# Kernel tuning notes

Hardware: AMD Instinct MI355X
Metric: run time of the kernel (lower is better)

Reference implementation:

```python
import jax, jax.numpy as jnp
import numpy as np

# ROIAlign config (torchvision semantics, aligned=False)
SPATIAL_SCALE = 0.25
POOLED = 7
SAMPLING_RATIO = 2
MODE = "max"  # from __init__ mode='max'


def setup_inputs() -> dict:
    key = jax.random.key(0)
    kf, kcx, kcy, kw, kh, kb = jax.random.split(key, 6)
    B, C, H, W = 2, 256, 200, 304
    N = 512
    IMG_H, IMG_W = H / SPATIAL_SCALE, W / SPATIAL_SCALE
    feature = jax.random.normal(kf, (B, C, H, W), dtype=jnp.float32)
    cx = jax.random.uniform(kcx, (N,)) * IMG_W
    cy = jax.random.uniform(kcy, (N,)) * IMG_H
    bw = jax.random.uniform(kw, (N,)) * 192.0 + 16.0
    bh = jax.random.uniform(kh, (N,)) * 192.0 + 16.0
    x1 = jnp.clip(cx - bw * 0.5, 0.0, IMG_W - 2.0)
    y1 = jnp.clip(cy - bh * 0.5, 0.0, IMG_H - 2.0)
    x2 = jnp.clip(cx + bw * 0.5, x1 + 1.0, IMG_W - 1.0)
    y2 = jnp.clip(cy + bh * 0.5, y1 + 1.0, IMG_H - 1.0)
    boxes = jnp.stack([x1, y1, x2, y2], axis=1).astype(jnp.float32)
    batch_idx = jax.random.randint(kb, (N,), 0, B, dtype=jnp.int32)
    return {"feature": feature, "boxes": boxes, "batch_idx": batch_idx}


def _sample_coords(start, size):
    # start,size: [N]; returns [N, POOLED*SAMPLING_RATIO] sample coordinates
    bin_sz = size / POOLED                         # [N]
    p = jnp.arange(POOLED, dtype=jnp.float32)      # bin index
    s = (jnp.arange(SAMPLING_RATIO, dtype=jnp.float32) + 0.5) / SAMPLING_RATIO
    # coord = start + (p + s) * bin_sz  -> [N, POOLED, RATIO]
    c = start[:, None, None] + (p[None, :, None] + s[None, None, :]) * bin_sz[:, None, None]
    return c.reshape(c.shape[0], POOLED * SAMPLING_RATIO)


def roi_align(feature, boxes, batch_idx):
    B, C, H, W = feature.shape
    roi = boxes * SPATIAL_SCALE                    # [N,4] in feature coords
    rs_x, rs_y, re_x, re_y = roi[:, 0], roi[:, 1], roi[:, 2], roi[:, 3]
    roi_w = jnp.maximum(re_x - rs_x, 1.0)
    roi_h = jnp.maximum(re_y - rs_y, 1.0)
    ys = _sample_coords(rs_y, roi_h)               # [N, Sy]
    xs = _sample_coords(rs_x, roi_w)               # [N, Sx]
    y = jnp.broadcast_to(ys[:, :, None], (ys.shape[0], ys.shape[1], xs.shape[1]))
    x = jnp.broadcast_to(xs[:, None, :], y.shape)  # [N, Sy, Sx]

    valid = (y > -1.0) & (y < H) & (x > -1.0) & (x < W)
    y = jnp.clip(y, 0.0, H - 1)
    x = jnp.clip(x, 0.0, W - 1)
    y0 = jnp.floor(y).astype(jnp.int32)
    x0 = jnp.floor(x).astype(jnp.int32)
    y1 = jnp.minimum(y0 + 1, H - 1)
    x1 = jnp.minimum(x0 + 1, W - 1)
    ly = y - y0.astype(y.dtype)
    lx = x - x0.astype(x.dtype)
    hy, hx = 1.0 - ly, 1.0 - lx
    b = batch_idx[:, None, None]
    # advanced indexing -> [N, Sy, Sx, C]
    val = (hy * hx)[..., None] * feature[b, :, y0, x0] \
        + (hy * lx)[..., None] * feature[b, :, y0, x1] \
        + (ly * hx)[..., None] * feature[b, :, y1, x0] \
        + (ly * lx)[..., None] * feature[b, :, y1, x1]
    val = jnp.where(valid[..., None], val, 0.0)
    N = boxes.shape[0]
    val = val.reshape(N, POOLED, SAMPLING_RATIO, POOLED, SAMPLING_RATIO, C)
    if MODE == "max":
        out = val.max(axis=(2, 4))                 # [N, PH, PW, C]
    else:
        out = val.mean(axis=(2, 4))
    return jnp.transpose(out, (0, 3, 1, 2))        # [N, C, PH, PW]


def reference(feature, boxes, batch_idx):
    return roi_align(feature, boxes, batch_idx)
```

## Files before the change

### kernel.cpp

```cpp
#include <hip/hip_runtime.h>


#define SPATIAL_SCALE 0.25f
#define POOLED 7
#define SR 2

constexpr int Bc = 2;
constexpr int Cc = 256;
constexpr int Hc = 200;
constexpr int Wc = 304;
constexpr int Nc = 512;

constexpr int CG      = 4;
constexpr int NSAMP   = POOLED * SR;
constexpr int NROW    = NSAMP * 2;
constexpr int XPAD    = 68;
constexpr int CH_STR  = NROW * XPAD;
constexpr int CELLS   = POOLED * POOLED;
constexpr int OUTS    = CG * CELLS;
constexpr int PER_BOX = Cc * CELLS;
constexpr int PLANE   = Hc * Wc;

constexpr int TB_F  = 1216;
constexpr int A_OFF = 784;
constexpr int R_OFF = 1176;
constexpr int X_OFF = 1204;
constexpr size_t TABLE_BYTES = (size_t)Nc * TB_F * sizeof(float);

__global__ __launch_bounds__(64) void roi_precompute_kernel(
    const float* __restrict__ boxes,
    float*       __restrict__ table)
{
    const int n   = blockIdx.x;
    const int tid = threadIdx.x;

    const float rsx = boxes[n * 4 + 0] * SPATIAL_SCALE;
    const float rsy = boxes[n * 4 + 1] * SPATIAL_SCALE;
    const float rex = boxes[n * 4 + 2] * SPATIAL_SCALE;
    const float rey = boxes[n * 4 + 3] * SPATIAL_SCALE;
    const float roi_w = fmaxf(rex - rsx, 1.0f);
    const float roi_h = fmaxf(rey - rsy, 1.0f);
    const float bin_w = roi_w / (float)POOLED;
    const float bin_h = roi_h / (float)POOLED;
    const float x_first = __fadd_rn(rsx, __fmul_rn(0.25f, bin_w));
    const float xc0     = fminf(fmaxf(x_first, 0.0f), (float)(Wc - 1));
    const int   xbase   = ((int)floorf(xc0)) & ~3;

    float* tb = table + (size_t)n * TB_F;
    int*   ti = (int*)tb;

    if (tid < CELLS) {
        const int ph = tid / POOLED;
        const int pw = tid - ph * POOLED;
        #pragma unroll
        for (int sy = 0; sy < SR; ++sy) {
            const int   sY  = ph * SR + sy;
            const float py  = (float)ph + ((float)sy + 0.5f) * 0.5f;
            const float fy  = __fadd_rn(rsy, __fmul_rn(py, bin_h));
            const bool  vy  = (fy > -1.0f) && (fy < (float)Hc);
            const float fyc = fminf(fmaxf(fy, 0.0f), (float)(Hc - 1));
            const int   y0i = (int)floorf(fyc);
            const float ly  = fyc - (float)y0i;
            const float hy  = 1.0f - ly;
            #pragma unroll
            for (int sx = 0; sx < SR; ++sx) {
                const float px  = (float)pw + ((float)sx + 0.5f) * 0.5f;
                const float fx  = __fadd_rn(rsx, __fmul_rn(px, bin_w));
                const bool  vx  = (fx > -1.0f) && (fx < (float)Wc);
                const float fxc = fminf(fmaxf(fx, 0.0f), (float)(Wc - 1));
                const int   x0i = (int)floorf(fxc);
                const float lx  = fxc - (float)x0i;
                const float hx  = 1.0f - lx;
                const int   c0  = x0i - xbase;
                const bool  v   = vy && vx;
                float4 w;
                w.x = v ? hy * hx : 0.0f;
                w.y = v ? hy * lx : 0.0f;
                w.z = v ? ly * hx : 0.0f;
                w.w = v ? ly * lx : 0.0f;
                const int tap = sy * SR + sx;
                ((float4*)tb)[tid * 4 + tap] = w;
                ti[A_OFF + tid * 8 + tap * 2 + 0] = sY * XPAD + c0;
                ti[A_OFF + tid * 8 + tap * 2 + 1] = (NSAMP + sY) * XPAD + c0;
            }
        }
    }
    if (tid < NROW) {
        const int which = tid / NSAMP;
        const int s     = tid - which * NSAMP;
        const int p     = s >> 1;
        const int sub   = s & 1;
        const float py  = (float)p + ((float)sub + 0.5f) * 0.5f;
        const float fy  = __fadd_rn(rsy, __fmul_rn(py, bin_h));
        const float fyc = fminf(fmaxf(fy, 0.0f), (float)(Hc - 1));
        const int   y0  = (int)floorf(fyc);
        const int   row = which ? min(y0 + 1, Hc - 1) : y0;
        ti[R_OFF + tid] = row * Wc;
    }
    if (tid == 0) ti[X_OFF] = xbase;
}

__global__ __launch_bounds__(256) void roi_align_main_kernel(
    const float* __restrict__ feature,
    const int*   __restrict__ batch_idx,
    const float* __restrict__ table,
    float*       __restrict__ out)
{
    __shared__ float lds[CG * CH_STR];

    const int bid = blockIdx.x;
    const int cg  = bid / Nc;
    const int n   = bid - cg * Nc;
    const int tid = threadIdx.x;

    const float* tb = table + (size_t)n * TB_F;
    const int*   ti = (const int*)tb;

    const int b     = batch_idx[n];
    const int xbase = ti[X_OFF];

    const int c_st   = tid >> 6;
    const int lane16 = tid & 15;
    const int rquad  = (tid >> 4) & 3;
    const int col    = min(xbase + lane16 * 4, Wc - 4);

    int roff[7];
    #pragma unroll
    for (int it = 0; it < 7; ++it)
        roff[it] = ti[R_OFF + it * 4 + rquad];

    const int cellc = min(tid, OUTS - 1);
    const int c_cl  = cellc / CELLS;
    const int cell  = cellc - c_cl * CELLS;
    const float4* wp = (const float4*)tb + (size_t)cell * 4;
    const float4 wv0 = wp[0], wv1 = wp[1], wv2 = wp[2], wv3 = wp[3];
    const int4* ap = (const int4*)(ti + A_OFF) + (size_t)cell * 2;
    const int4 av0 = ap[0], av1 = ap[1];

    const float* __restrict__ gbase =
        feature + ((size_t)b * Cc + (size_t)cg * CG + c_st) * (size_t)PLANE;
    float4 st[7];
    #pragma unroll
    for (int it = 0; it < 7; ++it)
        st[it] = *(const float4*)(gbase + roff[it] + col);

    const int lw = c_st * CH_STR + rquad * XPAD + lane16 * 4;
    #pragma unroll
    for (int it = 0; it < 7; ++it)
        *(float4*)&lds[lw + it * (4 * XPAD)] = st[it];

    __syncthreads();

    if (tid < OUTS) {
        const int lbase = c_cl * CH_STR;
        float m = -INFINITY;
        {   const int a0 = av0.x + lbase, a1 = av0.y + lbase;
            const float bil = wv0.x * lds[a0] + wv0.y * lds[a0 + 1]
                            + wv0.z * lds[a1] + wv0.w * lds[a1 + 1];
            m = fmaxf(m, bil); }
        {   const int a0 = av0.z + lbase, a1 = av0.w + lbase;
            const float bil = wv1.x * lds[a0] + wv1.y * lds[a0 + 1]
                            + wv1.z * lds[a1] + wv1.w * lds[a1 + 1];
            m = fmaxf(m, bil); }
        {   const int a0 = av1.x + lbase, a1 = av1.y + lbase;
            const float bil = wv2.x * lds[a0] + wv2.y * lds[a0 + 1]
                            + wv2.z * lds[a1] + wv2.w * lds[a1 + 1];
            m = fmaxf(m, bil); }
        {   const int a0 = av1.z + lbase, a1 = av1.w + lbase;
            const float bil = wv3.x * lds[a0] + wv3.y * lds[a0 + 1]
                            + wv3.z * lds[a1] + wv3.w * lds[a1 + 1];
            m = fmaxf(m, bil); }
        out[(size_t)n * PER_BOX + cg * OUTS + tid] = m;
    }
}

__global__ __launch_bounds__(256) void roi_align_max_fallback(
    const float* __restrict__ feature,
    const float* __restrict__ boxes,
    const int*   __restrict__ batch_idx,
    float*       __restrict__ out)
{
    __shared__ float lds[CG * CH_STR];

    int bid = blockIdx.x;
    int cg  = bid / Nc;
    int n   = bid - cg * Nc;
    int tid = threadIdx.x;

    float rsx = boxes[n * 4 + 0] * SPATIAL_SCALE;
    float rsy = boxes[n * 4 + 1] * SPATIAL_SCALE;
    float rex = boxes[n * 4 + 2] * SPATIAL_SCALE;
    float rey = boxes[n * 4 + 3] * SPATIAL_SCALE;
    float roi_w = fmaxf(rex - rsx, 1.0f);
    float roi_h = fmaxf(rey - rsy, 1.0f);
    float bin_w = roi_w / (float)POOLED;
    float bin_h = roi_h / (float)POOLED;
    int b = batch_idx[n];

    float x_first = __fadd_rn(rsx, __fmul_rn(0.25f, bin_w));
    float xc0 = fminf(fmaxf(x_first, 0.0f), (float)(Wc - 1));
    int xbase = ((int)floorf(xc0)) & ~3;

    const float* __restrict__ gbase =
        feature + ((size_t)b * Cc + (size_t)cg * CG) * (size_t)PLANE;

    int lane16 = tid & 15;
    int rbase  = tid >> 4;
    #pragma unroll
    for (int it = 0; it < 7; ++it) {
        int r       = it * 16 + rbase;
        int c_local = r / NROW;
        int slot    = r - c_local * NROW;
        int s       = slot % NSAMP;
        int which   = slot / NSAMP;
        int p       = s >> 1;
        int sub     = s & 1;
        float py = (float)p + ((float)sub + 0.5f) * 0.5f;
        float fy = __fadd_rn(rsy, __fmul_rn(py, bin_h));
        float fyc = fminf(fmaxf(fy, 0.0f), (float)(Hc - 1));
        int y0 = (int)floorf(fyc);
        int row = which ? min(y0 + 1, Hc - 1) : y0;
        int colf = min(xbase + lane16 * 4, Wc - 4);
        const float4 v = *(const float4*)(gbase + (size_t)c_local * PLANE
                                          + row * Wc + colf);
        *(float4*)&lds[c_local * CH_STR + slot * XPAD + lane16 * 4] = v;
    }
    __syncthreads();

    if (tid < OUTS) {
        int c_local = tid / CELLS;
        int cell    = tid - c_local * CELLS;
        int ph      = cell / POOLED;
        int pw      = cell - ph * POOLED;
        const float* __restrict__ L = &lds[c_local * CH_STR];

        float m = -INFINITY;
        #pragma unroll
        for (int sy = 0; sy < SR; ++sy) {
            int sY = ph * SR + sy;
            float py = (float)ph + ((float)sy + 0.5f) * 0.5f;
            float fy = __fadd_rn(rsy, __fmul_rn(py, bin_h));
            bool vy = (fy > -1.0f) && (fy < (float)Hc);
            float fyc = fminf(fmaxf(fy, 0.0f), (float)(Hc - 1));
            int y0 = (int)floorf(fyc);
            float ly = fyc - (float)y0;
            float hy = 1.0f - ly;
            const float* __restrict__ r0 = L + sY * XPAD;
            const float* __restrict__ r1 = L + (NSAMP + sY) * XPAD;

            #pragma unroll
            for (int sx = 0; sx < SR; ++sx) {
                float px = (float)pw + ((float)sx + 0.5f) * 0.5f;
                float fx = __fadd_rn(rsx, __fmul_rn(px, bin_w));
                bool vx = (fx > -1.0f) && (fx < (float)Wc);
                float fxc = fminf(fmaxf(fx, 0.0f), (float)(Wc - 1));
                int x0 = (int)floorf(fxc);
                float lx = fxc - (float)x0;
                float hx = 1.0f - lx;
                int c0 = x0 - xbase;

                float v00 = r0[c0], v01 = r0[c0 + 1];
                float v10 = r1[c0], v11 = r1[c0 + 1];
                float bil = hy * hx * v00 + hy * lx * v01 +
                            ly * hx * v10 + ly * lx * v11;
                float v = (vy && vx) ? bil : 0.0f;
                m = fmaxf(m, v);
            }
        }
        out[(size_t)n * PER_BOX + cg * OUTS + tid] = m;
    }
}

extern "C" void kernel_launch(void* const* d_in, const int* in_sizes, int n_in,
                              void* d_out, int out_size, void* d_ws, size_t ws_size,
                              hipStream_t stream) {
    const float* feature   = (const float*)d_in[0];
    const float* boxes     = (const float*)d_in[1];
    const int*   batch_idx = (const int*)d_in[2];
    float*       out       = (float*)d_out;

    const int grid = (Cc / CG) * Nc;
    if (d_ws != nullptr && ws_size >= TABLE_BYTES) {
        float* table = (float*)d_ws;
        roi_precompute_kernel<<<Nc, 64, 0, stream>>>(boxes, table);
        roi_align_main_kernel<<<grid, 256, 0, stream>>>(feature, batch_idx,
                                                        table, out);
    } else {
        roi_align_max_fallback<<<grid, 256, 0, stream>>>(feature, boxes,
                                                         batch_idx, out);
    }
}
```

Measured before the change: 255.4 us.

## Load only needed feature columns per ROI and recompute row offsets in-block

The main kernel now computes the x-span each ROI actually touches and skips the global float4 loads for lanes beyond that span, so fewer feature bytes are fetched for narrow boxes. Row offsets are recomputed from the box into shared memory rather than read from the precomputed table. The LDS row pitch shrinks from 68 to 60 floats, and the block index decode uses shifts. This adds a second barrier and some per-block scalar math, and relies on the box span fitting in 60 columns.

```diff
diff --git a/kernel.cpp b/kernel.cpp
--- a/kernel.cpp
+++ b/kernel.cpp
@@ -14,7 +14,7 @@
 constexpr int CG      = 4;
 constexpr int NSAMP   = POOLED * SR;
 constexpr int NROW    = NSAMP * 2;
-constexpr int XPAD    = 68;
+constexpr int XPAD    = 60;
 constexpr int CH_STR  = NROW * XPAD;
 constexpr int CELLS   = POOLED * POOLED;
 constexpr int OUTS    = CG * CELLS;
@@ -88,9 +88,7 @@
     if (tid < NROW) {
         const int which = tid / NSAMP;
         const int s     = tid - which * NSAMP;
-        const int p     = s >> 1;
-        const int sub   = s & 1;
-        const float py  = (float)p + ((float)sub + 0.5f) * 0.5f;
+        const float py  = fmaf((float)s, 0.5f, 0.25f);
         const float fy  = __fadd_rn(rsy, __fmul_rn(py, bin_h));
         const float fyc = fminf(fmaxf(fy, 0.0f), (float)(Hc - 1));
         const int   y0  = (int)floorf(fyc);
@@ -102,33 +100,21 @@
 
 __global__ __launch_bounds__(256) void roi_align_main_kernel(
     const float* __restrict__ feature,
+    const float* __restrict__ boxes,
     const int*   __restrict__ batch_idx,
     const float* __restrict__ table,
     float*       __restrict__ out)
 {
     __shared__ float lds[CG * CH_STR];
+    __shared__ int   rowoff_sh[NROW];
 
     const int bid = blockIdx.x;
-    const int cg  = bid / Nc;
-    const int n   = bid - cg * Nc;
+    const int cg  = bid >> 9;
+    const int n   = bid & (Nc - 1);
     const int tid = threadIdx.x;
 
     const float* tb = table + (size_t)n * TB_F;
     const int*   ti = (const int*)tb;
-
-    const int b     = batch_idx[n];
-    const int xbase = ti[X_OFF];
-
-    const int c_st   = tid >> 6;
-    const int lane16 = tid & 15;
-    const int rquad  = (tid >> 4) & 3;
-    const int col    = min(xbase + lane16 * 4, Wc - 4);
-
-    int roff[7];
-    #pragma unroll
-    for (int it = 0; it < 7; ++it)
-        roff[it] = ti[R_OFF + it * 4 + rquad];
-
     const int cellc = min(tid, OUTS - 1);
     const int c_cl  = cellc / CELLS;
     const int cell  = cellc - c_cl * CELLS;
@@ -137,18 +123,60 @@
     const int4* ap = (const int4*)(ti + A_OFF) + (size_t)cell * 2;
     const int4 av0 = ap[0], av1 = ap[1];
 
-    const float* __restrict__ gbase =
+    const float rsx = boxes[n * 4 + 0] * SPATIAL_SCALE;
+    const float rsy = boxes[n * 4 + 1] * SPATIAL_SCALE;
+    const float rex = boxes[n * 4 + 2] * SPATIAL_SCALE;
+    const float rey = boxes[n * 4 + 3] * SPATIAL_SCALE;
+    const float roi_w = fmaxf(rex - rsx, 1.0f);
+    const float roi_h = fmaxf(rey - rsy, 1.0f);
+    const float bin_w = roi_w / (float)POOLED;
+    const float bin_h = roi_h / (float)POOLED;
+    const int   b     = batch_idx[n];
+
+    const float x_first = __fadd_rn(rsx, __fmul_rn(0.25f, bin_w));
+    const float xc0     = fminf(fmaxf(x_first, 0.0f), (float)(Wc - 1));
+    const int   xbase   = ((int)floorf(xc0)) & ~3;
+
+    const float x_last = __fadd_rn(rsx, __fmul_rn(6.75f, bin_w));
+    const float xlc    = fminf(fmaxf(x_last, 0.0f), (float)(Wc - 1));
+    const int   x0l    = (int)floorf(xlc);
+    const int   xlastc = min(x0l + 1, Wc - 1);
+    const int   span   = xlastc - xbase + 1;
+    const int   nl4    = (span + 4) >> 2;
+
+    if (tid < NROW) {
+        const int  which = tid >= NSAMP;
+        const int  s     = which ? tid - NSAMP : tid;
+        const float py   = fmaf((float)s, 0.5f, 0.25f);
+        const float fy   = __fadd_rn(rsy, __fmul_rn(py, bin_h));
+        const float fyc  = fminf(fmaxf(fy, 0.0f), (float)(Hc - 1));
+        const int   y0   = (int)floorf(fyc);
+        const int   row  = which ? min(y0 + 1, Hc - 1) : y0;
+        rowoff_sh[tid] = row * Wc;
+    }
+    __syncthreads();
+
+    const int c_st   = tid >> 6;
+    const int lane16 = tid & 15;
+    const int rquad  = (tid >> 4) & 3;
+    const float* __restrict__ gplane =
         feature + ((size_t)b * Cc + (size_t)cg * CG + c_st) * (size_t)PLANE;
-    float4 st[7];
-    #pragma unroll
-    for (int it = 0; it < 7; ++it)
-        st[it] = *(const float4*)(gbase + roff[it] + col);
-
-    const int lw = c_st * CH_STR + rquad * XPAD + lane16 * 4;
-    #pragma unroll
-    for (int it = 0; it < 7; ++it)
-        *(float4*)&lds[lw + it * (4 * XPAD)] = st[it];
-
+    const int col = min(xbase + lane16 * 4, Wc - 4);
+
+    if (lane16 < nl4) {
+        int ro[7];
+        #pragma unroll
+        for (int it = 0; it < 7; ++it)
+            ro[it] = rowoff_sh[it * 4 + rquad];
+        float4 st[7];
+        #pragma unroll
+        for (int it = 0; it < 7; ++it)
+            st[it] = *(const float4*)(gplane + ro[it] + col);
+        const int lw = c_st * CH_STR + rquad * XPAD + lane16 * 4;
+        #pragma unroll
+        for (int it = 0; it < 7; ++it)
+            *(float4*)&lds[lw + it * (4 * XPAD)] = st[it];
+    }
     __syncthreads();
 
     if (tid < OUTS) {
@@ -174,13 +202,16 @@
     }
 }
 
+constexpr int XPAD_FB   = 68;
+constexpr int CH_STR_FB = NROW * XPAD_FB;
+
 __global__ __launch_bounds__(256) void roi_align_max_fallback(
     const float* __restrict__ feature,
     const float* __restrict__ boxes,
     const int*   __restrict__ batch_idx,
     float*       __restrict__ out)
 {
-    __shared__ float lds[CG * CH_STR];
+    __shared__ float lds[CG * CH_STR_FB];
 
     int bid = blockIdx.x;
     int cg  = bid / Nc;
@@ -213,9 +244,7 @@
         int slot    = r - c_local * NROW;
         int s       = slot % NSAMP;
         int which   = slot / NSAMP;
-        int p       = s >> 1;
-        int sub     = s & 1;
-        float py = (float)p + ((float)sub + 0.5f) * 0.5f;
+        float py = fmaf((float)s, 0.5f, 0.25f);
         float fy = __fadd_rn(rsy, __fmul_rn(py, bin_h));
         float fyc = fminf(fmaxf(fy, 0.0f), (float)(Hc - 1));
         int y0 = (int)floorf(fyc);
@@ -223,7 +252,7 @@
         int colf = min(xbase + lane16 * 4, Wc - 4);
         const float4 v = *(const float4*)(gbase + (size_t)c_local * PLANE
                                           + row * Wc + colf);
-        *(float4*)&lds[c_local * CH_STR + slot * XPAD + lane16 * 4] = v;
+        *(float4*)&lds[c_local * CH_STR_FB + slot * XPAD_FB + lane16 * 4] = v;
     }
     __syncthreads();
 
@@ -232,7 +261,7 @@
         int cell    = tid - c_local * CELLS;
         int ph      = cell / POOLED;
         int pw      = cell - ph * POOLED;
-        const float* __restrict__ L = &lds[c_local * CH_STR];
+        const float* __restrict__ L = &lds[c_local * CH_STR_FB];
 
         float m = -INFINITY;
         #pragma unroll
@@ -245,8 +274,8 @@
             int y0 = (int)floorf(fyc);
             float ly = fyc - (float)y0;
             float hy = 1.0f - ly;
-            const float* __restrict__ r0 = L + sY * XPAD;
-            const float* __restrict__ r1 = L + (NSAMP + sY) * XPAD;
+            const float* __restrict__ r0 = L + sY * XPAD_FB;
+            const float* __restrict__ r1 = L + (NSAMP + sY) * XPAD_FB;
 
             #pragma unroll
             for (int sx = 0; sx < SR; ++sx) {
@@ -283,8 +312,8 @@
     if (d_ws != nullptr && ws_size >= TABLE_BYTES) {
         float* table = (float*)d_ws;
         roi_precompute_kernel<<<Nc, 64, 0, stream>>>(boxes, table);
-        roi_align_main_kernel<<<grid, 256, 0, stream>>>(feature, batch_idx,
-                                                        table, out);
+        roi_align_main_kernel<<<grid, 256, 0, stream>>>(feature, boxes,
+                                                        batch_idx, table, out);
     } else {
         roi_align_max_fallback<<<grid, 256, 0, stream>>>(feature, boxes,
                                                          batch_idx, out);
```

New measurement: 236.5 us. -7.4%, faster.
